# Performance work log

Hardware: AMD Instinct MI355X
Metric: run time of the kernel (lower is better)

Reference implementation:

```python
import jax, jax.numpy as jnp
import numpy as np

B, C_IN, C_OUT, K, H, W_DIM, F_IN = 16, 64, 64, 3, 128, 128, 16
NKW = C_OUT * C_IN * K * K  # 36864 kernel weights per sample


def setup_inputs() -> dict:
    key = jax.random.key(0)
    ks = jax.random.split(key, 8)
    s = 0.05
    return {
        "x": jax.random.normal(ks[0], (B, C_IN, H, W_DIM), dtype=jnp.float32),
        "z": jax.random.normal(ks[1], (B, F_IN), dtype=jnp.float32),
        "W0": jax.random.normal(ks[2], (20, F_IN), dtype=jnp.float32) * s,
        "b0": jax.random.normal(ks[3], (20,), dtype=jnp.float32) * s,
        "W1": jax.random.normal(ks[4], (30, 20), dtype=jnp.float32) * s,
        "b1": jax.random.normal(ks[5], (30,), dtype=jnp.float32) * s,
        "W2": jax.random.normal(ks[6], (NKW + C_OUT, 30), dtype=jnp.float32) * s,
        "b2": jax.random.normal(ks[7], (NKW + C_OUT,), dtype=jnp.float32) * s,
    }


def reference(x, z, W0, b0, W1, b1, W2, b2):
    # Manifold MLP: ReLU after EVERY layer, including the final one (as in original code).
    h = jax.nn.relu(z @ W0.T + b0)
    h = jax.nn.relu(h @ W1.T + b1)
    aw = jax.nn.relu(h @ W2.T + b2)  # [B, NKW + C_OUT]

    kernels = aw[:, :NKW].reshape(B, C_OUT, C_IN, K, K)  # per-sample OIHW kernels
    biases = aw[:, NKW:]  # [B, C_OUT]

    def conv_one(xi, wi, bi):
        # xi: [C_IN, H, W], wi: [C_OUT, C_IN, K, K], bi: [C_OUT]
        y = jax.lax.conv_general_dilated(
            xi[None], wi, window_strides=(1, 1), padding="SAME",
            dimension_numbers=("NCHW", "OIHW", "NCHW"))[0]
        return y + bi[:, None, None]

    out = jax.vmap(conv_one)(x, kernels, biases)  # [B, C_OUT, H, W]
    return jax.nn.relu(out)
```

## Files before the change

kernel.cpp:

```cpp
#include <hip/hip_runtime.h>


typedef __bf16 bf16;
typedef __bf16 bf16x8 __attribute__((ext_vector_type(8)));
typedef float f32x4 __attribute__((ext_vector_type(4)));

#define NB 16
#define CI 64
#define CO 64
#define HH 128
#define WW 128
#define TS 16
#define HALO 18
#define NPL (HALO * HALO)
#define NKW 36864
#define NROWS 36928
#define WT2_BYTES ((size_t)NB * 9 * 4096 * 2)

__global__ __launch_bounds__(256)
void hyper_kernel(const float* __restrict__ z, const float* __restrict__ W0,
                  const float* __restrict__ b0, const float* __restrict__ W1,
                  const float* __restrict__ b1, const float* __restrict__ W2,
                  const float* __restrict__ b2, bf16* __restrict__ wt2,
                  float* __restrict__ biases) {
  __shared__ float h1s[NB][30];
  const int tid = threadIdx.x;
  if (tid < NB) {
    float h0[20];
    #pragma unroll
    for (int i = 0; i < 20; ++i) {
      float s = b0[i];
      #pragma unroll
      for (int j = 0; j < 16; ++j) s += W0[i * 16 + j] * z[tid * 16 + j];
      h0[i] = fmaxf(s, 0.f);
    }
    #pragma unroll
    for (int i = 0; i < 30; ++i) {
      float s = b1[i];
      #pragma unroll
      for (int j = 0; j < 20; ++j) s += W1[i * 20 + j] * h0[j];
      h1s[tid][i] = fmaxf(s, 0.f);
    }
  }
  __syncthreads();
  const int r = blockIdx.x * 256 + tid;
  if (r >= NROWS) return;
  float w2r[30];
  #pragma unroll
  for (int j = 0; j < 30; ++j) w2r[j] = W2[r * 30 + j];
  const float bb = b2[r];
  const bool isk = r < NKW;
  size_t base = 0;
  if (isk) {
    const int co = r / 576;
    const int rem = r - co * 576;
    const int ci = rem / 9;
    const int tap = rem - ci * 9;
    const int g = co >> 4, mm = co & 15;
    const int kh = ci >> 5, qq = (ci >> 3) & 3, jj = ci & 7;
    base = (size_t)(tap * 8 + g * 2 + kh) * 512 + (size_t)(qq * 16 + mm) * 8 + jj;
  }
  for (int b = 0; b < NB; ++b) {
    float s = bb;
    #pragma unroll
    for (int j = 0; j < 30; ++j) s += w2r[j] * h1s[b][j];
    s = fmaxf(s, 0.f);
    if (isk)
      wt2[(size_t)b * (9 * 4096) + base] = (bf16)s;
    else
      biases[b * CO + (r - NKW)] = s;
  }
}

__global__ __launch_bounds__(512, 4)
void conv_kernel(const float* __restrict__ x, const bf16* __restrict__ wt2,
                 const float* __restrict__ bias, float* __restrict__ out) {
  __shared__ __align__(16) bf16 xt[NPL * 64];

  const int b = blockIdx.z;
  const int x0 = blockIdx.x * TS;
  const int y0 = blockIdx.y * TS;
  const int tid = threadIdx.x;
  const int lane = tid & 63;
  const int wv = tid >> 6;
  const int m = lane & 15;
  const int q = lane >> 4;

  const char* wbase = (const char*)wt2 + (size_t)b * (9 * 8192) + lane * 16;

  bf16x8 abuf[2][4][2];
  #pragma unroll
  for (int i = 0; i < 4; ++i)
    #pragma unroll
    for (int kh = 0; kh < 2; ++kh)
      abuf[0][i][kh] =
          *reinterpret_cast<const bf16x8*>(wbase + (i * 2 + kh) * 1024);

  for (int it = tid; it < NPL * 8; it += 512) {
    const int cig = ((it >> 2) * 810) >> 16;
    const int pl = it - cig * 324;
    const int py = (pl * 57) >> 10;
    const int px = pl - py * 18;
    const int gy = y0 + py - 1, gx = x0 + px - 1;
    const bool inb = ((unsigned)gy < (unsigned)HH) & ((unsigned)gx < (unsigned)WW);
    bf16x8 v8;
    #pragma unroll
    for (int j = 0; j < 8; ++j) v8[j] = (bf16)0.f;
    if (inb) {
      const float* src =
          x + ((size_t)(b * CI + cig * 8) << 14) + (size_t)(gy * WW + gx);
      #pragma unroll
      for (int j = 0; j < 8; ++j) v8[j] = (bf16)src[(size_t)j << 14];
    }
    *reinterpret_cast<bf16x8*>(reinterpret_cast<char*>(xt) + (pl << 7) +
                               ((cig ^ (pl & 7)) << 4)) = v8;
  }

  f32x4 acc[4][2];
  #pragma unroll
  for (int i = 0; i < 4; ++i) {
    acc[i][0] = (f32x4){0.f, 0.f, 0.f, 0.f};
    acc[i][1] = (f32x4){0.f, 0.f, 0.f, 0.f};
  }

  const int ty0 = wv * 2;

  __syncthreads();

  #pragma unroll
  for (int tap = 0; tap < 9; ++tap) {
    const int cur = tap & 1, nxt = cur ^ 1;
    if (tap < 8) {
      const char* wt_n = wbase + (tap + 1) * 8192;
      #pragma unroll
      for (int i = 0; i < 4; ++i)
        #pragma unroll
        for (int kh = 0; kh < 2; ++kh)
          abuf[nxt][i][kh] =
              *reinterpret_cast<const bf16x8*>(wt_n + (i * 2 + kh) * 1024);
    }
    const int dy = (tap * 11) >> 5;
    const int dx = tap - dy * 3;
    const int plb = (ty0 + dy) * 18 + dx + m;
    __builtin_amdgcn_s_setprio(1);
    #pragma unroll
    for (int kh = 0; kh < 2; ++kh) {
      const int qk = q + kh * 4;
      #pragma unroll
      for (int j = 0; j < 2; ++j) {
        const int pl = plb + j * 18;
        const bf16x8 bv = *reinterpret_cast<const bf16x8*>(
            reinterpret_cast<const char*>(xt) + (pl << 7) +
            ((qk ^ (pl & 7)) << 4));
        #pragma unroll
        for (int i = 0; i < 4; ++i)
          acc[i][j] = __builtin_amdgcn_mfma_f32_16x16x32_bf16(
              abuf[cur][i][kh], bv, acc[i][j], 0, 0, 0);
      }
    }
    __builtin_amdgcn_s_setprio(0);
  }

  const float* bp = bias + b * CO;
  float* ob = out + ((size_t)(b * CO) << 14) + (size_t)((y0 + ty0) * WW + x0 + m);
  #pragma unroll
  for (int i = 0; i < 4; ++i)
    #pragma unroll
    for (int j = 0; j < 2; ++j)
      #pragma unroll
      for (int r = 0; r < 4; ++r) {
        const int co = i * 16 + q * 4 + r;
        float v = acc[i][j][r] + bp[co];
        ob[((size_t)co << 14) + j * WW] = fmaxf(v, 0.f);
      }
}

extern "C" void kernel_launch(void* const* d_in, const int* in_sizes, int n_in,
                              void* d_out, int out_size, void* d_ws,
                              size_t ws_size, hipStream_t stream) {
  const float* x = (const float*)d_in[0];
  const float* z = (const float*)d_in[1];
  const float* W0 = (const float*)d_in[2];
  const float* b0 = (const float*)d_in[3];
  const float* W1 = (const float*)d_in[4];
  const float* b1 = (const float*)d_in[5];
  const float* W2 = (const float*)d_in[6];
  const float* b2 = (const float*)d_in[7];
  float* out = (float*)d_out;

  bf16* wt2 = (bf16*)d_ws;
  float* biases = (float*)((char*)d_ws + WT2_BYTES);

  hipLaunchKernelGGL(hyper_kernel, dim3((NROWS + 255) / 256), dim3(256), 0,
                     stream, z, W0, b0, W1, b1, W2, b2, wt2, biases);
  hipLaunchKernelGGL(conv_kernel, dim3(WW / TS, HH / TS, NB), dim3(512), 0,
                     stream, x, wt2, biases, out);
}
```

Measured before the change: 183.7 us.

## Batch halo loads into registers and remap blocks across XCDs

The halo-tile load loop now issues all six iterations' global loads up front into a register buffer, using clamped addresses and a validity mask, before converting to bf16 and writing to LDS. This raises memory-level parallelism in place of serialized load-then-store iterations. The grid is flattened to 1D with a block-id swizzle so that consecutive blocks dispatched to the same XCD share a sample, which is meant to improve L2 reuse of weights and input. It costs extra registers (48 floats per thread), which may pressure occupancy under launch_bounds(512,4).

```diff
diff --git a/kernel.cpp b/kernel.cpp
--- a/kernel.cpp
+++ b/kernel.cpp
@@ -77,9 +77,11 @@
                  const float* __restrict__ bias, float* __restrict__ out) {
   __shared__ __align__(16) bf16 xt[NPL * 64];
 
-  const int b = blockIdx.z;
-  const int x0 = blockIdx.x * TS;
-  const int y0 = blockIdx.y * TS;
+  const int id = (blockIdx.x & 7) * 128 + (blockIdx.x >> 3);
+  const int b = id >> 6;
+  const int x0 = (id & 7) * TS;
+  const int y0 = ((id >> 3) & 7) * TS;
+
   const int tid = threadIdx.x;
   const int lane = tid & 63;
   const int wv = tid >> 6;
@@ -96,24 +98,37 @@
       abuf[0][i][kh] =
           *reinterpret_cast<const bf16x8*>(wbase + (i * 2 + kh) * 1024);
 
-  for (int it = tid; it < NPL * 8; it += 512) {
+  const float* xb = x + ((size_t)b << 20);
+  float vbuf[6][8];
+  int pls[6], cigs[6];
+  bool inbs[6];
+  #pragma unroll
+  for (int t = 0; t < 6; ++t) {
+    const int it = min(tid + t * 512, NPL * 8 - 1);
     const int cig = ((it >> 2) * 810) >> 16;
     const int pl = it - cig * 324;
     const int py = (pl * 57) >> 10;
     const int px = pl - py * 18;
-    const int gy = y0 + py - 1, gx = x0 + px - 1;
-    const bool inb = ((unsigned)gy < (unsigned)HH) & ((unsigned)gx < (unsigned)WW);
+    int gy = y0 + py - 1, gx = x0 + px - 1;
+    inbs[t] = ((unsigned)gy < (unsigned)HH) & ((unsigned)gx < (unsigned)WW);
+    gy = min(max(gy, 0), HH - 1);
+    gx = min(max(gx, 0), WW - 1);
+    pls[t] = pl;
+    cigs[t] = cig;
+    const float* src = xb + ((size_t)cig << 17) + (gy << 7) + gx;
+    #pragma unroll
+    for (int j = 0; j < 8; ++j) vbuf[t][j] = src[(size_t)j << 14];
+  }
+
+  #pragma unroll
+  for (int t = 0; t < 6; ++t) {
+    if (t == 5 && tid >= NPL * 8 - 5 * 512) break;
     bf16x8 v8;
     #pragma unroll
-    for (int j = 0; j < 8; ++j) v8[j] = (bf16)0.f;
-    if (inb) {
-      const float* src =
-          x + ((size_t)(b * CI + cig * 8) << 14) + (size_t)(gy * WW + gx);
-      #pragma unroll
-      for (int j = 0; j < 8; ++j) v8[j] = (bf16)src[(size_t)j << 14];
-    }
-    *reinterpret_cast<bf16x8*>(reinterpret_cast<char*>(xt) + (pl << 7) +
-                               ((cig ^ (pl & 7)) << 4)) = v8;
+    for (int j = 0; j < 8; ++j)
+      v8[j] = inbs[t] ? (bf16)vbuf[t][j] : (bf16)0.f;
+    *reinterpret_cast<bf16x8*>(reinterpret_cast<char*>(xt) + (pls[t] << 7) +
+                               ((cigs[t] ^ (pls[t] & 7)) << 4)) = v8;
   }
 
   f32x4 acc[4][2];
@@ -193,6 +208,6 @@
 
   hipLaunchKernelGGL(hyper_kernel, dim3((NROWS + 255) / 256), dim3(256), 0,
                      stream, z, W0, b0, W1, b1, W2, b2, wt2, biases);
-  hipLaunchKernelGGL(conv_kernel, dim3(WW / TS, HH / TS, NB), dim3(512), 0,
-                     stream, x, wt2, biases, out);
+  hipLaunchKernelGGL(conv_kernel, dim3(1024), dim3(512), 0, stream, x, wt2,
+                     biases, out);
 }
```

Result: faster. 179.4 us (-2.3%).

## Restage conv input via per-channel vector row loads with 32x8 tiles and XCD-aware block order

Applied to the files above, without the earlier changes.

The conv kernel now uses 32x8 output tiles instead of 16x16. The input halo is staged differently: each lane owns one input channel and reads whole rows with float4 loads into registers, instead of eight strided scalar loads across channels per pixel. It then writes bf16 scalars into the swizzled LDS tile. A 1D grid with an XCD-style remap of block IDs keeps blocks of the same batch together, for better L2 reuse of weights and input. The trade-offs are many 2-byte LDS stores, lanes whose global addresses are 64KB apart within each load instruction, and higher register pressure from the 80-float staging buffers.

```diff
diff --git a/kernel.cpp b/kernel.cpp
--- a/kernel.cpp
+++ b/kernel.cpp
@@ -10,12 +10,12 @@
 #define CO 64
 #define HH 128
 #define WW 128
-#define TS 16
-#define HALO 18
-#define NPL (HALO * HALO)
 #define NKW 36864
 #define NROWS 36928
 #define WT2_BYTES ((size_t)NB * 9 * 4096 * 2)
+
+typedef const __attribute__((address_space(1))) void* gas_ptr;
+typedef __attribute__((address_space(3))) void* las_ptr;
 
 __global__ __launch_bounds__(256)
 void hyper_kernel(const float* __restrict__ z, const float* __restrict__ W0,
@@ -73,21 +73,51 @@
 }
 
 __global__ __launch_bounds__(512, 4)
-void conv_kernel(const float* __restrict__ x, const bf16* __restrict__ wt2,
-                 const float* __restrict__ bias, float* __restrict__ out) {
-  __shared__ __align__(16) bf16 xt[NPL * 64];
-
-  const int b = blockIdx.z;
-  const int x0 = blockIdx.x * TS;
-  const int y0 = blockIdx.y * TS;
+void conv_fused(const float* __restrict__ x, const bf16* __restrict__ wt2,
+                const float* __restrict__ bias, float* __restrict__ out) {
+  __shared__ __align__(16) bf16 xt[360 * 64];
+
+  const int id = (blockIdx.x & 7) * 128 + (blockIdx.x >> 3);
+  const int b = id >> 6;
+  const int rem = id & 63;
+  const int x0 = (rem & 3) * 32;
+  const int y0 = (rem >> 2) * 8;
+
   const int tid = threadIdx.x;
   const int lane = tid & 63;
   const int wv = tid >> 6;
   const int m = lane & 15;
   const int q = lane >> 4;
 
-  const char* wbase = (const char*)wt2 + (size_t)b * (9 * 8192) + lane * 16;
-
+  const int ci = lane;
+  const float* xrow = x + (((size_t)b * CI + ci) << 14);
+  const int gyA = y0 - 1 + wv;
+  const int gyB = gyA + 8;
+  const bool vA = (gyA >= 0) && (gyA < HH);
+  const bool doB = (wv < 2);
+  const bool vB = doB && (gyB < HH);
+
+  float va[40], vb[40];
+  if (vA) {
+    const float* s = xrow + ((size_t)gyA << 7);
+    #pragma unroll
+    for (int jj = 0; jj < 10; ++jj) {
+      const int bpx = min(max(x0 - 4 + 4 * jj, 0), WW - 4);
+      *reinterpret_cast<f32x4*>(&va[4 * jj]) =
+          *reinterpret_cast<const f32x4*>(s + bpx);
+    }
+  }
+  if (vB) {
+    const float* s = xrow + ((size_t)gyB << 7);
+    #pragma unroll
+    for (int jj = 0; jj < 10; ++jj) {
+      const int bpx = min(max(x0 - 4 + 4 * jj, 0), WW - 4);
+      *reinterpret_cast<f32x4*>(&vb[4 * jj]) =
+          *reinterpret_cast<const f32x4*>(s + bpx);
+    }
+  }
+
+  const char* wbase = (const char*)wt2 + (size_t)b * 73728 + lane * 16;
   bf16x8 abuf[2][4][2];
   #pragma unroll
   for (int i = 0; i < 4; ++i)
@@ -96,24 +126,30 @@
       abuf[0][i][kh] =
           *reinterpret_cast<const bf16x8*>(wbase + (i * 2 + kh) * 1024);
 
-  for (int it = tid; it < NPL * 8; it += 512) {
-    const int cig = ((it >> 2) * 810) >> 16;
-    const int pl = it - cig * 324;
-    const int py = (pl * 57) >> 10;
-    const int px = pl - py * 18;
-    const int gy = y0 + py - 1, gx = x0 + px - 1;
-    const bool inb = ((unsigned)gy < (unsigned)HH) & ((unsigned)gx < (unsigned)WW);
-    bf16x8 v8;
-    #pragma unroll
-    for (int j = 0; j < 8; ++j) v8[j] = (bf16)0.f;
-    if (inb) {
-      const float* src =
-          x + ((size_t)(b * CI + cig * 8) << 14) + (size_t)(gy * WW + gx);
-      #pragma unroll
-      for (int j = 0; j < 8; ++j) v8[j] = (bf16)src[(size_t)j << 14];
-    }
-    *reinterpret_cast<bf16x8*>(reinterpret_cast<char*>(xt) + (pl << 7) +
-                               ((cig ^ (pl & 7)) << 4)) = v8;
+  const bool zlo = (x0 == 0);
+  const bool zhi = (x0 == 96);
+  const int gq = ci >> 3, bo = (ci & 7) << 1;
+  {
+    const int py = wv;
+    #pragma unroll
+    for (int pxl = 0; pxl < 34; ++pxl) {
+      bf16 v = (bf16)0.f;
+      if (vA && !(pxl == 0 && zlo) && !(pxl == 33 && zhi)) v = (bf16)va[pxl + 3];
+      const int pl = py * 36 + pxl;
+      *reinterpret_cast<bf16*>(reinterpret_cast<char*>(xt) + (pl << 7) +
+                               ((gq ^ (pl & 7)) << 4) + bo) = v;
+    }
+  }
+  if (doB) {
+    const int py = wv + 8;
+    #pragma unroll
+    for (int pxl = 0; pxl < 34; ++pxl) {
+      bf16 v = (bf16)0.f;
+      if (vB && !(pxl == 0 && zlo) && !(pxl == 33 && zhi)) v = (bf16)vb[pxl + 3];
+      const int pl = py * 36 + pxl;
+      *reinterpret_cast<bf16*>(reinterpret_cast<char*>(xt) + (pl << 7) +
+                               ((gq ^ (pl & 7)) << 4) + bo) = v;
+    }
   }
 
   f32x4 acc[4][2];
@@ -122,8 +158,6 @@
     acc[i][0] = (f32x4){0.f, 0.f, 0.f, 0.f};
     acc[i][1] = (f32x4){0.f, 0.f, 0.f, 0.f};
   }
-
-  const int ty0 = wv * 2;
 
   __syncthreads();
 
@@ -141,37 +175,37 @@
     }
     const int dy = (tap * 11) >> 5;
     const int dx = tap - dy * 3;
-    const int plb = (ty0 + dy) * 18 + dx + m;
+    const int plb = (wv + dy) * 36 + dx + m;
     __builtin_amdgcn_s_setprio(1);
     #pragma unroll
     for (int kh = 0; kh < 2; ++kh) {
       const int qk = q + kh * 4;
       #pragma unroll
-      for (int j = 0; j < 2; ++j) {
-        const int pl = plb + j * 18;
+      for (int n = 0; n < 2; ++n) {
+        const int pl = plb + n * 16;
         const bf16x8 bv = *reinterpret_cast<const bf16x8*>(
             reinterpret_cast<const char*>(xt) + (pl << 7) +
             ((qk ^ (pl & 7)) << 4));
         #pragma unroll
         for (int i = 0; i < 4; ++i)
-          acc[i][j] = __builtin_amdgcn_mfma_f32_16x16x32_bf16(
-              abuf[cur][i][kh], bv, acc[i][j], 0, 0, 0);
+          acc[i][n] = __builtin_amdgcn_mfma_f32_16x16x32_bf16(
+              abuf[cur][i][kh], bv, acc[i][n], 0, 0, 0);
       }
     }
     __builtin_amdgcn_s_setprio(0);
   }
 
   const float* bp = bias + b * CO;
-  float* ob = out + ((size_t)(b * CO) << 14) + (size_t)((y0 + ty0) * WW + x0 + m);
+  float* ob = out + ((size_t)(b * CO) << 14) + (size_t)((y0 + wv) * WW + x0 + m);
   #pragma unroll
   for (int i = 0; i < 4; ++i)
     #pragma unroll
-    for (int j = 0; j < 2; ++j)
+    for (int n = 0; n < 2; ++n)
       #pragma unroll
       for (int r = 0; r < 4; ++r) {
         const int co = i * 16 + q * 4 + r;
-        float v = acc[i][j][r] + bp[co];
-        ob[((size_t)co << 14) + j * WW] = fmaxf(v, 0.f);
+        float v = acc[i][n][r] + bp[co];
+        ob[((size_t)co << 14) + n * 16] = fmaxf(v, 0.f);
       }
 }
 
@@ -193,6 +227,6 @@
 
   hipLaunchKernelGGL(hyper_kernel, dim3((NROWS + 255) / 256), dim3(256), 0,
                      stream, z, W0, b0, W1, b1, W2, b2, wt2, biases);
-  hipLaunchKernelGGL(conv_kernel, dim3(WW / TS, HH / TS, NB), dim3(512), 0,
-                     stream, x, wt2, biases, out);
+  hipLaunchKernelGGL(conv_fused, dim3(1024), dim3(512), 0, stream, x, wt2,
+                     biases, out);
 }
```

New measurement: 176.8 us. -3.7%, faster.
